# Kernel optimization log

Hardware: AMD Instinct MI355X
Metric: run time of the kernel (lower is better)

## Reference

```python
import jax, jax.numpy as jnp
import numpy as np

B, S, D = 2, 2048, 1024
H = 16
HD = D // H
MINUS_INFINITY = -1000000000.0


def setup_inputs() -> dict:
    key = jax.random.key(0)
    ks = jax.random.split(key, 6)
    sc = 0.02
    return {
        "x": jax.random.normal(ks[0], (B, S, D), dtype=jnp.float32),
        "Wq": jax.random.normal(ks[1], (D, D), dtype=jnp.float32) * sc,
        "Wk": jax.random.normal(ks[2], (D, D), dtype=jnp.float32) * sc,
        "Wv": jax.random.normal(ks[3], (D, D), dtype=jnp.float32) * sc,
        "Wo": jax.random.normal(ks[4], (D, D), dtype=jnp.float32) * sc,
        "bo": jnp.zeros((D,), dtype=jnp.float32),
    }


def reference(x, Wq, Wk, Wv, Wo, bo):
    b, n, _ = x.shape
    # Linear with transpose_b=True: x @ W.T
    q = jnp.einsum('bnd,ed->bne', x, Wq).reshape(b, n, H, HD).transpose(0, 2, 1, 3)
    k = jnp.einsum('bnd,ed->bne', x, Wk).reshape(b, n, H, HD).transpose(0, 2, 1, 3)
    v = jnp.einsum('bnd,ed->bne', x, Wv).reshape(b, n, H, HD).transpose(0, 2, 1, 3)
    scores = jnp.einsum('bhqd,bhkd->bhqk', q, k) * (1.0 / HD ** 0.5)
    mask = jnp.triu(jnp.ones((n, n), dtype=scores.dtype), k=1) * MINUS_INFINITY
    scores = scores + mask[None, None, :, :]
    attn = jax.nn.softmax(scores, axis=-1)  # dropout prob = 0.0
    ctx = jnp.einsum('bhqk,bhkd->bhqd', attn, v)
    ctx = ctx.transpose(0, 2, 1, 3).reshape(b, n, D)
    return jnp.einsum('bnd,ed->bne', ctx, Wo) + bo
```

## Files before the change

### kernel.cpp

```cpp
#include <hip/hip_runtime.h>
#include <hip/hip_bf16.h>

#define B_  2
#define S_  2048
#define D_  1024
#define H_  16
#define HD_ 64

typedef __attribute__((ext_vector_type(8))) short short8;
typedef __attribute__((ext_vector_type(4))) float f32x4;

__device__ __forceinline__ unsigned short f2b(float f) {
    __hip_bfloat16 h = __float2bfloat16(f);
    unsigned short u;
    __builtin_memcpy(&u, &h, 2);
    return u;
}

__global__ __launch_bounds__(256) void convert_kernel(
    const float* __restrict__ x,  const float* __restrict__ Wq,
    const float* __restrict__ Wk, const float* __restrict__ Wv,
    const float* __restrict__ Wo, unsigned short* __restrict__ dst)
{
    const long long i4 = blockIdx.x * 256 + threadIdx.x;
    const long long e  = i4 * 4;
    const long long M1 = 1048576LL;
    const float* src;
    if      (e < 4 * M1) src = x  + e;
    else if (e < 5 * M1) src = Wq + (e - 4 * M1);
    else if (e < 6 * M1) src = Wk + (e - 5 * M1);
    else if (e < 7 * M1) src = Wv + (e - 6 * M1);
    else                 src = Wo + (e - 7 * M1);
    float4 v = *(const float4*)src;
    unsigned long long pk = (unsigned long long)f2b(v.x)
                          | ((unsigned long long)f2b(v.y) << 16)
                          | ((unsigned long long)f2b(v.z) << 32)
                          | ((unsigned long long)f2b(v.w) << 48);
    *(unsigned long long*)&dst[e] = pk;
}

__global__ __launch_bounds__(256) void qkv_proj_kernel(
    const unsigned short* __restrict__ x,
    const unsigned short* __restrict__ Wq,
    const unsigned short* __restrict__ Wk,
    const unsigned short* __restrict__ Wv,
    unsigned short* __restrict__ q_ws,
    unsigned short* __restrict__ k_ws,
    unsigned short* __restrict__ vT_ws)
{
    __shared__ unsigned short a_lds[128][72];
    __shared__ unsigned short b_lds[128][72];

    const int m0 = blockIdx.x * 128;
    const int n0 = blockIdx.y * 128;
    const int which = blockIdx.z;
    const unsigned short* W = (which == 0) ? Wq : (which == 1) ? Wk : Wv;

    const int tid  = threadIdx.x;
    const int wave = tid >> 6;
    const int lane = tid & 63;
    const int l15  = lane & 15;
    const int quad = lane >> 4;
    const int wm = (wave & 1) * 64;
    const int wn = (wave >> 1) * 64;

    f32x4 acc[4][4];
    #pragma unroll
    for (int sm = 0; sm < 4; ++sm)
        #pragma unroll
        for (int sn = 0; sn < 4; ++sn)
            #pragma unroll
            for (int r = 0; r < 4; ++r) acc[sm][sn][r] = 0.f;

    const int row = tid >> 3;
    const int c8  = tid & 7;

    for (int kk = 0; kk < D_; kk += 64) {
        #pragma unroll
        for (int rp = 0; rp < 4; ++rp) {
            *(uint4*)&a_lds[row + rp * 32][c8 * 8] =
                *(const uint4*)&x[(m0 + row + rp * 32) * D_ + kk + c8 * 8];
            *(uint4*)&b_lds[row + rp * 32][c8 * 8] =
                *(const uint4*)&W[(n0 + row + rp * 32) * D_ + kk + c8 * 8];
        }
        __syncthreads();
        #pragma unroll
        for (int kc = 0; kc < 2; ++kc) {
            short8 af[4], bf[4];
            #pragma unroll
            for (int s = 0; s < 4; ++s) {
                af[s] = *(const short8*)&a_lds[wm + s * 16 + l15][kc * 32 + quad * 8];
                bf[s] = *(const short8*)&b_lds[wn + s * 16 + l15][kc * 32 + quad * 8];
            }
            #pragma unroll
            for (int sm = 0; sm < 4; ++sm)
                #pragma unroll
                for (int sn = 0; sn < 4; ++sn)
                    acc[sm][sn] = __builtin_amdgcn_mfma_f32_16x16x32_bf16(
                        af[sm], bf[sn], acc[sm][sn], 0, 0, 0);
        }
        __syncthreads();
    }

    #pragma unroll
    for (int sm = 0; sm < 4; ++sm) {
        #pragma unroll
        for (int sn = 0; sn < 4; ++sn) {
            const int n  = n0 + wn + sn * 16 + l15;
            const int h  = n >> 6;
            const int hd = n & 63;
            const int mbase = m0 + wm + sm * 16 + quad * 4;
            const int b     = mbase >> 11;
            const int sbase = mbase & 2047;
            if (which == 2) {
                unsigned long long pk = 0;
                #pragma unroll
                for (int r = 0; r < 4; ++r)
                    pk |= (unsigned long long)f2b(acc[sm][sn][r]) << (16 * r);
                *(unsigned long long*)&vT_ws[((b * H_ + h) * HD_ + hd) * S_ + sbase] = pk;
            } else if (which == 0) {
                #pragma unroll
                for (int r = 0; r < 4; ++r)
                    q_ws[((b * H_ + h) * S_ + (sbase + r)) * HD_ + hd] =
                        f2b(acc[sm][sn][r] * 0.125f);
            } else {
                #pragma unroll
                for (int r = 0; r < 4; ++r)
                    k_ws[((b * H_ + h) * S_ + (sbase + r)) * HD_ + hd] =
                        f2b(acc[sm][sn][r]);
            }
        }
    }
}

__global__ __launch_bounds__(256) void attn_kernel(
    const unsigned short* __restrict__ q_ws,
    const unsigned short* __restrict__ k_ws,
    const unsigned short* __restrict__ vT_ws,
    unsigned short* __restrict__ ctx_ws)
{
    __shared__ unsigned short k_lds[2][64][72];
    __shared__ unsigned short vT_lds[2][64][72];

    const int pair = blockIdx.x;
    const int bh   = blockIdx.y;

    const int tid  = threadIdx.x;
    const int wave = tid >> 6;
    const int lane = tid & 63;
    const int l15  = lane & 15;
    const int quad = lane >> 4;
    const int row  = tid >> 3;
    const int c8   = tid & 7;

    const unsigned short* Qh = q_ws + bh * (S_ * HD_);
    const unsigned short* Kh = k_ws + bh * (S_ * HD_);
    const unsigned short* Vt = vT_ws + bh * (HD_ * S_);
    const int b = bh >> 4;
    const int h = bh & 15;

    const int src0 = l15 + 32 * (quad & 1);
    const int src1 = src0 + 16;
    const int sel  = quad >> 1;

    #pragma unroll
    for (int ph = 0; ph < 2; ++ph) {
        const int qt = (ph == 0) ? (31 - pair) : pair;
        const int q0 = qt * 64;
        const int qg = q0 + wave * 16 + l15;

        __syncthreads();
        *(uint4*)&k_lds[0][row][c8 * 8]       = *(const uint4*)&Kh[row * HD_ + c8 * 8];
        *(uint4*)&k_lds[0][row + 32][c8 * 8]  = *(const uint4*)&Kh[(row + 32) * HD_ + c8 * 8];
        *(uint4*)&vT_lds[0][row][c8 * 8]      = *(const uint4*)&Vt[row * S_ + c8 * 8];
        *(uint4*)&vT_lds[0][row + 32][c8 * 8] = *(const uint4*)&Vt[(row + 32) * S_ + c8 * 8];

        short8 aq[2];
        aq[0] = *(const short8*)&Qh[qg * HD_ + quad * 8];
        aq[1] = *(const short8*)&Qh[qg * HD_ + 32 + quad * 8];

        __syncthreads();

        float l_lane = 0.f;
        f32x4 o[4];
        #pragma unroll
        for (int f = 0; f < 4; ++f)
            #pragma unroll
            for (int r = 0; r < 4; ++r) o[f][r] = 0.f;

        for (int kt = 0; kt <= qt; ++kt) {
            const int cur = kt & 1;
            if (kt < qt) {
                const int nk0 = (kt + 1) * 64;
                const int nb  = cur ^ 1;
                *(uint4*)&k_lds[nb][row][c8 * 8]       = *(const uint4*)&Kh[(nk0 + row) * HD_ + c8 * 8];
                *(uint4*)&k_lds[nb][row + 32][c8 * 8]  = *(const uint4*)&Kh[(nk0 + row + 32) * HD_ + c8 * 8];
                *(uint4*)&vT_lds[nb][row][c8 * 8]      = *(const uint4*)&Vt[row * S_ + nk0 + c8 * 8];
                *(uint4*)&vT_lds[nb][row + 32][c8 * 8] = *(const uint4*)&Vt[(row + 32) * S_ + nk0 + c8 * 8];
            }

            f32x4 sc[4];
            #pragma unroll
            for (int f = 0; f < 4; ++f)
                #pragma unroll
                for (int r = 0; r < 4; ++r) sc[f][r] = 0.f;
            #pragma unroll
            for (int f = 0; f < 4; ++f)
                #pragma unroll
                for (int kc = 0; kc < 2; ++kc) {
                    short8 ak = *(const short8*)&k_lds[cur][f * 16 + l15][kc * 32 + quad * 8];
                    sc[f] = __builtin_amdgcn_mfma_f32_16x16x32_bf16(ak, aq[kc], sc[f], 0, 0, 0);
                }

            float p[4][4];
            if (kt == qt) {
                const int kbase = kt * 64 + quad * 4;
                #pragma unroll
                for (int f = 0; f < 4; ++f)
                    #pragma unroll
                    for (int r = 0; r < 4; ++r) {
                        const float pv = __expf(sc[f][r]);
                        p[f][r] = (kbase + f * 16 + r > qg) ? 0.f : pv;
                        l_lane += p[f][r];
                    }
            } else {
                #pragma unroll
                for (int f = 0; f < 4; ++f)
                    #pragma unroll
                    for (int r = 0; r < 4; ++r) {
                        p[f][r] = __expf(sc[f][r]);
                        l_lane += p[f][r];
                    }
            }

            unsigned int pd[4][2];
            #pragma unroll
            for (int f = 0; f < 4; ++f) {
                pd[f][0] = (unsigned int)f2b(p[f][0]) | ((unsigned int)f2b(p[f][1]) << 16);
                pd[f][1] = (unsigned int)f2b(p[f][2]) | ((unsigned int)f2b(p[f][3]) << 16);
            }

            #pragma unroll
            for (int c = 0; c < 2; ++c) {
                const int a0 = __shfl((int)pd[c * 2][0],     src0, 64);
                const int a1 = __shfl((int)pd[c * 2][1],     src0, 64);
                const int a2 = __shfl((int)pd[c * 2][0],     src1, 64);
                const int a3 = __shfl((int)pd[c * 2][1],     src1, 64);
                const int b0 = __shfl((int)pd[c * 2 + 1][0], src0, 64);
                const int b1 = __shfl((int)pd[c * 2 + 1][1], src0, 64);
                const int b2 = __shfl((int)pd[c * 2 + 1][0], src1, 64);
                const int b3 = __shfl((int)pd[c * 2 + 1][1], src1, 64);
                union { int i[4]; short8 s; } u2;
                u2.i[0] = sel ? b0 : a0;
                u2.i[1] = sel ? b1 : a1;
                u2.i[2] = sel ? b2 : a2;
                u2.i[3] = sel ? b3 : a3;
                #pragma unroll
                for (int f = 0; f < 4; ++f) {
                    short8 av = *(const short8*)&vT_lds[cur][f * 16 + l15][c * 32 + quad * 8];
                    o[f] = __builtin_amdgcn_mfma_f32_16x16x32_bf16(av, u2.s, o[f], 0, 0, 0);
                }
            }

            __syncthreads();
        }

        float l = l_lane;
        l += __shfl_xor(l, 16, 64);
        l += __shfl_xor(l, 32, 64);
        const float inv_l = 1.0f / l;

        #pragma unroll
        for (int f = 0; f < 4; ++f) {
            unsigned long long pk = 0;
            #pragma unroll
            for (int r = 0; r < 4; ++r)
                pk |= (unsigned long long)f2b(o[f][r] * inv_l) << (16 * r);
            *(unsigned long long*)&ctx_ws[(b * S_ + qg) * D_ + h * 64 + f * 16 + quad * 4] = pk;
        }
    }
}

__global__ __launch_bounds__(256) void out_proj_kernel(
    const unsigned short* __restrict__ ctx,
    const unsigned short* __restrict__ Wo,
    const float* __restrict__ bo,
    float* __restrict__ out)
{
    __shared__ unsigned short a_lds[128][72];
    __shared__ unsigned short b_lds[128][72];

    const int m0 = blockIdx.x * 128;
    const int n0 = blockIdx.y * 128;

    const int tid  = threadIdx.x;
    const int wave = tid >> 6;
    const int lane = tid & 63;
    const int l15  = lane & 15;
    const int quad = lane >> 4;
    const int wm = (wave & 1) * 64;
    const int wn = (wave >> 1) * 64;

    f32x4 acc[4][4];
    #pragma unroll
    for (int sm = 0; sm < 4; ++sm)
        #pragma unroll
        for (int sn = 0; sn < 4; ++sn)
            #pragma unroll
            for (int r = 0; r < 4; ++r) acc[sm][sn][r] = 0.f;

    const int row = tid >> 3;
    const int c8  = tid & 7;

    for (int kk = 0; kk < D_; kk += 64) {
        #pragma unroll
        for (int rp = 0; rp < 4; ++rp) {
            *(uint4*)&a_lds[row + rp * 32][c8 * 8] =
                *(const uint4*)&ctx[(m0 + row + rp * 32) * D_ + kk + c8 * 8];
            *(uint4*)&b_lds[row + rp * 32][c8 * 8] =
                *(const uint4*)&Wo[(n0 + row + rp * 32) * D_ + kk + c8 * 8];
        }
        __syncthreads();
        #pragma unroll
        for (int kc = 0; kc < 2; ++kc) {
            short8 af[4], bf[4];
            #pragma unroll
            for (int s = 0; s < 4; ++s) {
                af[s] = *(const short8*)&a_lds[wm + s * 16 + l15][kc * 32 + quad * 8];
                bf[s] = *(const short8*)&b_lds[wn + s * 16 + l15][kc * 32 + quad * 8];
            }
            #pragma unroll
            for (int sm = 0; sm < 4; ++sm)
                #pragma unroll
                for (int sn = 0; sn < 4; ++sn)
                    acc[sm][sn] = __builtin_amdgcn_mfma_f32_16x16x32_bf16(
                        af[sm], bf[sn], acc[sm][sn], 0, 0, 0);
        }
        __syncthreads();
    }

    #pragma unroll
    for (int sm = 0; sm < 4; ++sm) {
        #pragma unroll
        for (int sn = 0; sn < 4; ++sn) {
            const int n = n0 + wn + sn * 16 + l15;
            const float bias = bo[n];
            const int mbase = m0 + wm + sm * 16 + quad * 4;
            #pragma unroll
            for (int r = 0; r < 4; ++r)
                out[(mbase + r) * D_ + n] = acc[sm][sn][r] + bias;
        }
    }
}

extern "C" void kernel_launch(void* const* d_in, const int* in_sizes, int n_in,
                              void* d_out, int out_size, void* d_ws, size_t ws_size,
                              hipStream_t stream) {
    const float* x  = (const float*)d_in[0];
    const float* Wq = (const float*)d_in[1];
    const float* Wk = (const float*)d_in[2];
    const float* Wv = (const float*)d_in[3];
    const float* Wo = (const float*)d_in[4];
    const float* bo = (const float*)d_in[5];
    float* out = (float*)d_out;

    const size_t M1 = 1048576;
    const size_t SZ = 4 * M1;

    unsigned short* xb  = (unsigned short*)d_ws;
    unsigned short* wqb = xb  + SZ;
    unsigned short* wkb = wqb + M1;
    unsigned short* wvb = wkb + M1;
    unsigned short* wob = wvb + M1;
    unsigned short* q_ws   = wob + M1;
    unsigned short* k_ws   = q_ws + SZ;
    unsigned short* vT_ws  = k_ws + SZ;
    unsigned short* ctx_ws = vT_ws + SZ;

    convert_kernel<<<dim3(8192), 256, 0, stream>>>(x, Wq, Wk, Wv, Wo, xb);
    qkv_proj_kernel<<<dim3(32, 8, 3), 256, 0, stream>>>(xb, wqb, wkb, wvb, q_ws, k_ws, vT_ws);
    attn_kernel<<<dim3(16, 32), 256, 0, stream>>>(q_ws, k_ws, vT_ws, ctx_ws);
    out_proj_kernel<<<dim3(32, 8), 256, 0, stream>>>(ctx_ws, wob, bo, out);
}
```

Baseline: 190.6 us.

## Load K and V fragments directly from global memory instead of LDS staging

```diff
diff --git a/kernel.cpp b/kernel.cpp
--- a/kernel.cpp
+++ b/kernel.cpp
@@ -139,9 +139,6 @@
     const unsigned short* __restrict__ vT_ws,
     unsigned short* __restrict__ ctx_ws)
 {
-    __shared__ unsigned short k_lds[2][64][72];
-    __shared__ unsigned short vT_lds[2][64][72];
-
     const int pair = blockIdx.x;
     const int bh   = blockIdx.y;
 
@@ -150,8 +147,6 @@
     const int lane = tid & 63;
     const int l15  = lane & 15;
     const int quad = lane >> 4;
-    const int row  = tid >> 3;
-    const int c8   = tid & 7;
 
     const unsigned short* Qh = q_ws + bh * (S_ * HD_);
     const unsigned short* Kh = k_ws + bh * (S_ * HD_);
@@ -169,18 +164,10 @@
         const int q0 = qt * 64;
         const int qg = q0 + wave * 16 + l15;
 
-        __syncthreads();
-        *(uint4*)&k_lds[0][row][c8 * 8]       = *(const uint4*)&Kh[row * HD_ + c8 * 8];
-        *(uint4*)&k_lds[0][row + 32][c8 * 8]  = *(const uint4*)&Kh[(row + 32) * HD_ + c8 * 8];
-        *(uint4*)&vT_lds[0][row][c8 * 8]      = *(const uint4*)&Vt[row * S_ + c8 * 8];
-        *(uint4*)&vT_lds[0][row + 32][c8 * 8] = *(const uint4*)&Vt[(row + 32) * S_ + c8 * 8];
-
         short8 aq[2];
         aq[0] = *(const short8*)&Qh[qg * HD_ + quad * 8];
         aq[1] = *(const short8*)&Qh[qg * HD_ + 32 + quad * 8];
 
-        __syncthreads();
-
         float l_lane = 0.f;
         f32x4 o[4];
         #pragma unroll
@@ -189,15 +176,19 @@
             for (int r = 0; r < 4; ++r) o[f][r] = 0.f;
 
         for (int kt = 0; kt <= qt; ++kt) {
-            const int cur = kt & 1;
-            if (kt < qt) {
-                const int nk0 = (kt + 1) * 64;
-                const int nb  = cur ^ 1;
-                *(uint4*)&k_lds[nb][row][c8 * 8]       = *(const uint4*)&Kh[(nk0 + row) * HD_ + c8 * 8];
-                *(uint4*)&k_lds[nb][row + 32][c8 * 8]  = *(const uint4*)&Kh[(nk0 + row + 32) * HD_ + c8 * 8];
-                *(uint4*)&vT_lds[nb][row][c8 * 8]      = *(const uint4*)&Vt[row * S_ + nk0 + c8 * 8];
-                *(uint4*)&vT_lds[nb][row + 32][c8 * 8] = *(const uint4*)&Vt[(row + 32) * S_ + nk0 + c8 * 8];
-            }
+            const int k0 = kt * 64;
+
+            short8 ak[4][2], av[4][2];
+            #pragma unroll
+            for (int f = 0; f < 4; ++f)
+                #pragma unroll
+                for (int kc = 0; kc < 2; ++kc)
+                    ak[f][kc] = *(const short8*)&Kh[(k0 + f * 16 + l15) * HD_ + kc * 32 + quad * 8];
+            #pragma unroll
+            for (int f = 0; f < 4; ++f)
+                #pragma unroll
+                for (int c = 0; c < 2; ++c)
+                    av[f][c] = *(const short8*)&Vt[(f * 16 + l15) * S_ + k0 + c * 32 + quad * 8];
 
             f32x4 sc[4];
             #pragma unroll
@@ -207,14 +198,12 @@
             #pragma unroll
             for (int f = 0; f < 4; ++f)
                 #pragma unroll
-                for (int kc = 0; kc < 2; ++kc) {
-                    short8 ak = *(const short8*)&k_lds[cur][f * 16 + l15][kc * 32 + quad * 8];
-                    sc[f] = __builtin_amdgcn_mfma_f32_16x16x32_bf16(ak, aq[kc], sc[f], 0, 0, 0);
-                }
+                for (int kc = 0; kc < 2; ++kc)
+                    sc[f] = __builtin_amdgcn_mfma_f32_16x16x32_bf16(ak[f][kc], aq[kc], sc[f], 0, 0, 0);
 
             float p[4][4];
             if (kt == qt) {
-                const int kbase = kt * 64 + quad * 4;
+                const int kbase = k0 + quad * 4;
                 #pragma unroll
                 for (int f = 0; f < 4; ++f)
                     #pragma unroll
@@ -256,13 +245,9 @@
                 u2.i[2] = sel ? b2 : a2;
                 u2.i[3] = sel ? b3 : a3;
                 #pragma unroll
-                for (int f = 0; f < 4; ++f) {
-                    short8 av = *(const short8*)&vT_lds[cur][f * 16 + l15][c * 32 + quad * 8];
-                    o[f] = __builtin_amdgcn_mfma_f32_16x16x32_bf16(av, u2.s, o[f], 0, 0, 0);
-                }
-            }
-
-            __syncthreads();
+                for (int f = 0; f < 4; ++f)
+                    o[f] = __builtin_amdgcn_mfma_f32_16x16x32_bf16(av[f][c], u2.s, o[f], 0, 0, 0);
+            }
         }
 
         float l = l_lane;
```

Result: slower. 260.3 us (+36.6%).

## Split attention KV loop across two blocks and combine partial outputs

Applied to the files above, without the earlier changes.

```diff
diff --git a/kernel.cpp b/kernel.cpp
--- a/kernel.cpp
+++ b/kernel.cpp
@@ -15,6 +15,12 @@
     unsigned short u;
     __builtin_memcpy(&u, &h, 2);
     return u;
+}
+__device__ __forceinline__ float b2f(unsigned short u) {
+    unsigned int x = ((unsigned int)u) << 16;
+    float f;
+    __builtin_memcpy(&f, &x, 4);
+    return f;
 }
 
 __global__ __launch_bounds__(256) void convert_kernel(
@@ -137,13 +143,15 @@
     const unsigned short* __restrict__ q_ws,
     const unsigned short* __restrict__ k_ws,
     const unsigned short* __restrict__ vT_ws,
-    unsigned short* __restrict__ ctx_ws)
+    unsigned short* __restrict__ po,
+    float* __restrict__ pl)
 {
     __shared__ unsigned short k_lds[2][64][72];
     __shared__ unsigned short vT_lds[2][64][72];
 
-    const int pair = blockIdx.x;
-    const int bh   = blockIdx.y;
+    const int p     = blockIdx.x & 15;
+    const int sig   = blockIdx.x >> 4;
+    const int bh    = blockIdx.y;
 
     const int tid  = threadIdx.x;
     const int wave = tid >> 6;
@@ -159,21 +167,27 @@
     const int b = bh >> 4;
     const int h = bh & 15;
 
+    unsigned short* po_s = po + (size_t)sig * (B_ * S_ * D_);
+    float*          pl_s = pl + (size_t)sig * (B_ * S_ * H_);
+
     const int src0 = l15 + 32 * (quad & 1);
     const int src1 = src0 + 16;
     const int sel  = quad >> 1;
 
     #pragma unroll
     for (int ph = 0; ph < 2; ++ph) {
-        const int qt = (ph == 0) ? (31 - pair) : pair;
+        const int qt = (ph == 0) ? (31 - p) : p;
         const int q0 = qt * 64;
         const int qg = q0 + wave * 16 + l15;
 
         __syncthreads();
-        *(uint4*)&k_lds[0][row][c8 * 8]       = *(const uint4*)&Kh[row * HD_ + c8 * 8];
-        *(uint4*)&k_lds[0][row + 32][c8 * 8]  = *(const uint4*)&Kh[(row + 32) * HD_ + c8 * 8];
-        *(uint4*)&vT_lds[0][row][c8 * 8]      = *(const uint4*)&Vt[row * S_ + c8 * 8];
-        *(uint4*)&vT_lds[0][row + 32][c8 * 8] = *(const uint4*)&Vt[(row + 32) * S_ + c8 * 8];
+        if (sig <= qt) {
+            const int k0 = sig * 64;
+            *(uint4*)&k_lds[0][row][c8 * 8]       = *(const uint4*)&Kh[(k0 + row) * HD_ + c8 * 8];
+            *(uint4*)&k_lds[0][row + 32][c8 * 8]  = *(const uint4*)&Kh[(k0 + row + 32) * HD_ + c8 * 8];
+            *(uint4*)&vT_lds[0][row][c8 * 8]      = *(const uint4*)&Vt[row * S_ + k0 + c8 * 8];
+            *(uint4*)&vT_lds[0][row + 32][c8 * 8] = *(const uint4*)&Vt[(row + 32) * S_ + k0 + c8 * 8];
+        }
 
         short8 aq[2];
         aq[0] = *(const short8*)&Qh[qg * HD_ + quad * 8];
@@ -188,10 +202,10 @@
             #pragma unroll
             for (int r = 0; r < 4; ++r) o[f][r] = 0.f;
 
-        for (int kt = 0; kt <= qt; ++kt) {
-            const int cur = kt & 1;
-            if (kt < qt) {
-                const int nk0 = (kt + 1) * 64;
+        for (int kt = sig; kt <= qt; kt += 2) {
+            const int cur = ((kt - sig) >> 1) & 1;
+            if (kt + 2 <= qt) {
+                const int nk0 = (kt + 2) * 64;
                 const int nb  = cur ^ 1;
                 *(uint4*)&k_lds[nb][row][c8 * 8]       = *(const uint4*)&Kh[(nk0 + row) * HD_ + c8 * 8];
                 *(uint4*)&k_lds[nb][row + 32][c8 * 8]  = *(const uint4*)&Kh[(nk0 + row + 32) * HD_ + c8 * 8];
@@ -212,7 +226,7 @@
                     sc[f] = __builtin_amdgcn_mfma_f32_16x16x32_bf16(ak, aq[kc], sc[f], 0, 0, 0);
                 }
 
-            float p[4][4];
+            float pr[4][4];
             if (kt == qt) {
                 const int kbase = kt * 64 + quad * 4;
                 #pragma unroll
@@ -220,24 +234,24 @@
                     #pragma unroll
                     for (int r = 0; r < 4; ++r) {
                         const float pv = __expf(sc[f][r]);
-                        p[f][r] = (kbase + f * 16 + r > qg) ? 0.f : pv;
-                        l_lane += p[f][r];
+                        pr[f][r] = (kbase + f * 16 + r > qg) ? 0.f : pv;
+                        l_lane += pr[f][r];
                     }
             } else {
                 #pragma unroll
                 for (int f = 0; f < 4; ++f)
                     #pragma unroll
                     for (int r = 0; r < 4; ++r) {
-                        p[f][r] = __expf(sc[f][r]);
-                        l_lane += p[f][r];
+                        pr[f][r] = __expf(sc[f][r]);
+                        l_lane += pr[f][r];
                     }
             }
 
             unsigned int pd[4][2];
             #pragma unroll
             for (int f = 0; f < 4; ++f) {
-                pd[f][0] = (unsigned int)f2b(p[f][0]) | ((unsigned int)f2b(p[f][1]) << 16);
-                pd[f][1] = (unsigned int)f2b(p[f][2]) | ((unsigned int)f2b(p[f][3]) << 16);
+                pd[f][0] = (unsigned int)f2b(pr[f][0]) | ((unsigned int)f2b(pr[f][1]) << 16);
+                pd[f][1] = (unsigned int)f2b(pr[f][2]) | ((unsigned int)f2b(pr[f][3]) << 16);
             }
 
             #pragma unroll
@@ -268,17 +282,45 @@
         float l = l_lane;
         l += __shfl_xor(l, 16, 64);
         l += __shfl_xor(l, 32, 64);
-        const float inv_l = 1.0f / l;
+        const int rowg = b * S_ + qg;
+        if (quad == 0) pl_s[rowg * H_ + h] = l;
 
         #pragma unroll
         for (int f = 0; f < 4; ++f) {
             unsigned long long pk = 0;
             #pragma unroll
             for (int r = 0; r < 4; ++r)
-                pk |= (unsigned long long)f2b(o[f][r] * inv_l) << (16 * r);
-            *(unsigned long long*)&ctx_ws[(b * S_ + qg) * D_ + h * 64 + f * 16 + quad * 4] = pk;
-        }
-    }
+                pk |= (unsigned long long)f2b(o[f][r]) << (16 * r);
+            *(unsigned long long*)&po_s[rowg * D_ + h * 64 + f * 16 + quad * 4] = pk;
+        }
+    }
+}
+
+__global__ __launch_bounds__(256) void combine_kernel(
+    const unsigned short* __restrict__ po,
+    const float* __restrict__ pl,
+    unsigned short* __restrict__ ctx_ws)
+{
+    const int t = blockIdx.x * 256 + threadIdx.x;
+    const int e = t * 4;
+    const int rowg = e >> 10;
+    const int col  = e & 1023;
+    const int h    = col >> 6;
+
+    const float l = pl[rowg * H_ + h] + pl[(B_ * S_ * H_) + rowg * H_ + h];
+    const float inv_l = 1.0f / l;
+
+    const unsigned long long a = *(const unsigned long long*)&po[e];
+    const unsigned long long c = *(const unsigned long long*)&po[(size_t)(B_ * S_ * D_) + e];
+
+    unsigned long long pk = 0;
+    #pragma unroll
+    for (int r = 0; r < 4; ++r) {
+        const float o0 = b2f((unsigned short)(a >> (16 * r)));
+        const float o1 = b2f((unsigned short)(c >> (16 * r)));
+        pk |= (unsigned long long)f2b((o0 + o1) * inv_l) << (16 * r);
+    }
+    *(unsigned long long*)&ctx_ws[e] = pk;
 }
 
 __global__ __launch_bounds__(256) void out_proj_kernel(
@@ -376,9 +418,14 @@
     unsigned short* k_ws   = q_ws + SZ;
     unsigned short* vT_ws  = k_ws + SZ;
     unsigned short* ctx_ws = vT_ws + SZ;
+    unsigned short* po1    = ctx_ws + SZ;
+    float*          pl     = (float*)(po1 + SZ);
+    unsigned short* po = po1;
+    float* pl2 = (float*)(po + 2 * SZ);
 
     convert_kernel<<<dim3(8192), 256, 0, stream>>>(x, Wq, Wk, Wv, Wo, xb);
     qkv_proj_kernel<<<dim3(32, 8, 3), 256, 0, stream>>>(xb, wqb, wkb, wvb, q_ws, k_ws, vT_ws);
-    attn_kernel<<<dim3(16, 32), 256, 0, stream>>>(q_ws, k_ws, vT_ws, ctx_ws);
+    attn_kernel<<<dim3(32, 32), 256, 0, stream>>>(q_ws, k_ws, vT_ws, po, pl2);
+    combine_kernel<<<dim3(4096), 256, 0, stream>>>(po, pl2, ctx_ws);
     out_proj_kernel<<<dim3(32, 8), 256, 0, stream>>>(ctx_ws, wob, bo, out);
 }
```

New measurement: 191.9 us. About the same (+0.7%).
